# Kernel optimization log

Measured on AMD Instinct MI355X. Metric: run time of the kernel, lower is better.

The kernel has to match this reference:

```python
import jax, jax.numpy as jnp
import numpy as np

LN_EPS = 1e-5

def setup_inputs() -> dict:
    key = jax.random.key(0)
    ks = jax.random.split(key, 8)
    B, L, D, H = 4, 2048, 512, 8
    x = jax.random.normal(ks[0], (B, L, D), dtype=jnp.float32)
    token_ids = jax.random.randint(ks[1], (B, L), 0, 50000, dtype=jnp.int64)
    s = 1.0 / np.sqrt(D)
    Wq = jax.random.normal(ks[2], (D, D), dtype=jnp.float32) * s
    Wk = jax.random.normal(ks[3], (D, D), dtype=jnp.float32) * s
    Wv = jax.random.normal(ks[4], (D, D), dtype=jnp.float32) * s
    Wo = jax.random.normal(ks[5], (D, D), dtype=jnp.float32) * s
    gamma = jnp.ones((D,), dtype=jnp.float32)
    beta = jnp.zeros((D,), dtype=jnp.float32)
    return {"x": x, "token_ids": token_ids, "Wq": Wq, "Wk": Wk,
            "Wv": Wv, "Wo": Wo, "gamma": gamma, "beta": beta}

def reference(x, token_ids, Wq, Wk, Wv, Wo, gamma, beta):
    B, L, D = x.shape
    H = 8
    Dh = D // H
    residual = x
    # Pre-LN
    mu = jnp.mean(x, axis=-1, keepdims=True)
    var = jnp.mean(jnp.square(x - mu), axis=-1, keepdims=True)
    xn = (x - mu) * jax.lax.rsqrt(var + LN_EPS) * gamma + beta
    # projections (torch Linear: y = x @ W.T), split heads -> [B,H,L,Dh]
    def proj(W):
        return jnp.einsum('bld,ed->ble', xn, W).reshape(B, L, H, Dh).transpose(0, 2, 1, 3)
    Q, K, V = proj(Wq), proj(Wk), proj(Wv)
    scale = jnp.sqrt(jnp.float32(Dh))
    scores = jnp.einsum('bhqd,bhkd->bhqk', Q, K) / scale  # [B,H,L,L]
    neg_inf = jnp.float32(-jnp.inf)
    causal = jnp.triu(jnp.ones((L, L), dtype=bool), k=1)           # [L,L]
    pad = (token_ids == 0)[:, None, None, :]                       # [B,1,1,L]
    scores = jnp.where(causal[None, None], neg_inf, scores)
    scores = jnp.where(pad, neg_inf, scores)
    all_masked = jnp.all(jnp.isinf(scores), axis=-1, keepdims=True)
    scores = jnp.where(all_masked, 0.0, scores)
    attn = jax.nn.softmax(scores, axis=-1)  # dropout is identity in eval
    out = jnp.einsum('bhqk,bhkd->bhqd', attn, V)
    out = out.transpose(0, 2, 1, 3).reshape(B, L, D)
    out = jnp.einsum('bld,ed->ble', out, Wo)
    return residual + out
```

## Files before the change

kernel.cpp:

```cpp
#include <hip/hip_runtime.h>
#include <math.h>

typedef unsigned short u16;
typedef unsigned int u32;
typedef unsigned long long u64;
typedef float f32x4 __attribute__((ext_vector_type(4)));
typedef __bf16 bf16x8 __attribute__((ext_vector_type(8)));
typedef __bf16 bf16x4 __attribute__((ext_vector_type(4)));

constexpr int Bc = 4, Lc = 2048, Dc = 512, Hc = 8, DHc = 64;
constexpr int NTOK = Bc * Lc;
constexpr float LN_EPS = 1e-5f;
constexpr int KS = 72;
constexpr int PS = 72;
constexpr float QSCALE = 0.125f * 1.44269504088896340736f;
constexpr float MNEG = -1e30f;

__device__ inline u16 bf_bits(float f) {
  return __builtin_bit_cast(u16, (__bf16)f);
}

__global__ __launch_bounds__(256) void prep_kernel(const float* __restrict__ s0,
                                                   const float* __restrict__ s1,
                                                   const float* __restrict__ s2,
                                                   const float* __restrict__ s3,
                                                   u16* __restrict__ d0,
                                                   u16* __restrict__ d1,
                                                   u16* __restrict__ d2,
                                                   u16* __restrict__ d3,
                                                   const int* __restrict__ tok,
                                                   u64* __restrict__ pm) {
  int bid = blockIdx.x;
  if (bid < 1024) {
    int mat = bid >> 8;
    int i = ((bid & 255) * 256 + threadIdx.x) * 4;
    const float* s = (mat == 0) ? s0 : (mat == 1) ? s1 : (mat == 2) ? s2 : s3;
    u16* d = (mat == 0) ? d0 : (mat == 1) ? d1 : (mat == 2) ? d2 : d3;
    float4 v = *(const float4*)&s[i];
    bf16x4 o;
    o[0] = (__bf16)v.x; o[1] = (__bf16)v.y; o[2] = (__bf16)v.z; o[3] = (__bf16)v.w;
    *(bf16x4*)&d[i] = o;
  } else {
    int wid = ((bid - 1024) * 256 + threadIdx.x) >> 6;
    int lane = threadIdx.x & 63;
    u64 m = __ballot(tok[(size_t)wid * 64 + lane] == 0);
    if (lane == 0) pm[wid] = m;
  }
}

__global__ __launch_bounds__(256) void ln_kernel(const float* __restrict__ x,
                                                 const float* __restrict__ gamma,
                                                 const float* __restrict__ beta,
                                                 u16* __restrict__ xn) {
  int wave = threadIdx.x >> 6;
  int lane = threadIdx.x & 63;
  int row  = blockIdx.x * 4 + wave;
  const float* xr = x + (size_t)row * Dc;
  float4 v0 = ((const float4*)xr)[lane * 2];
  float4 v1 = ((const float4*)xr)[lane * 2 + 1];
  float sum = v0.x + v0.y + v0.z + v0.w + v1.x + v1.y + v1.z + v1.w;
  float sq  = v0.x*v0.x + v0.y*v0.y + v0.z*v0.z + v0.w*v0.w
            + v1.x*v1.x + v1.y*v1.y + v1.z*v1.z + v1.w*v1.w;
  #pragma unroll
  for (int off = 32; off > 0; off >>= 1) {
    sum += __shfl_xor(sum, off);
    sq  += __shfl_xor(sq, off);
  }
  float mu = sum * (1.0f / Dc);
  float rs = rsqrtf(sq * (1.0f / Dc) - mu * mu + LN_EPS);
  float4 g0 = ((const float4*)gamma)[lane * 2];
  float4 g1 = ((const float4*)gamma)[lane * 2 + 1];
  float4 b0 = ((const float4*)beta)[lane * 2];
  float4 b1 = ((const float4*)beta)[lane * 2 + 1];
  bf16x8 o;
  o[0] = (__bf16)((v0.x - mu) * rs * g0.x + b0.x);
  o[1] = (__bf16)((v0.y - mu) * rs * g0.y + b0.y);
  o[2] = (__bf16)((v0.z - mu) * rs * g0.z + b0.z);
  o[3] = (__bf16)((v0.w - mu) * rs * g0.w + b0.w);
  o[4] = (__bf16)((v1.x - mu) * rs * g1.x + b1.x);
  o[5] = (__bf16)((v1.y - mu) * rs * g1.y + b1.y);
  o[6] = (__bf16)((v1.z - mu) * rs * g1.z + b1.z);
  o[7] = (__bf16)((v1.w - mu) * rs * g1.w + b1.w);
  *(bf16x8*)&xn[(size_t)row * Dc + lane * 8] = o;
}

template <int MODE>
__global__ __launch_bounds__(256) void gemm_bf16(const u16* __restrict__ A,
                                                 const u16* __restrict__ W,
                                                 const float* __restrict__ res,
                                                 float* __restrict__ out_f,
                                                 u16* __restrict__ o_q,
                                                 u16* __restrict__ o_k,
                                                 u16* __restrict__ o_v,
                                                 float* __restrict__ vm) {
  __shared__ u16 As[128 * KS];
  __shared__ u16 Bs[128 * KS];
  int tid = threadIdx.x;
  int lane = tid & 63;
  int w = tid >> 6;
  int wr = w >> 1, wc = w & 1;
  int cc = lane & 15, rb = lane >> 4;
  int n0 = blockIdx.x * 128;
  int e0 = blockIdx.y * 128;
  f32x4 acc[4][4] = {};
  for (int k0 = 0; k0 < Dc; k0 += 64) {
    #pragma unroll
    for (int u = 0; u < 4; u++) {
      int idx = u * 256 + tid;
      int row = idx >> 3;
      int col = (idx & 7) << 3;
      *(uint4*)&As[row * KS + col] = *(const uint4*)&A[(size_t)(n0 + row) * Dc + k0 + col];
      *(uint4*)&Bs[row * KS + col] = *(const uint4*)&W[(size_t)(e0 + row) * Dc + k0 + col];
    }
    __syncthreads();
    #pragma unroll
    for (int kk = 0; kk < 64; kk += 32) {
      bf16x8 aF[4], bF[4];
      #pragma unroll
      for (int m = 0; m < 4; m++)
        aF[m] = *(bf16x8*)&As[(wr * 64 + m * 16 + cc) * KS + kk + rb * 8];
      #pragma unroll
      for (int n = 0; n < 4; n++)
        bF[n] = *(bf16x8*)&Bs[(wc * 64 + n * 16 + cc) * KS + kk + rb * 8];
      #pragma unroll
      for (int m = 0; m < 4; m++)
        #pragma unroll
        for (int n = 0; n < 4; n++)
          acc[m][n] = __builtin_amdgcn_mfma_f32_16x16x32_bf16(aF[m], bF[n], acc[m][n], 0, 0, 0);
    }
    __syncthreads();
  }
  if (MODE == 3) {
    int bb = n0 >> 11;
    int mat = e0 >> 9;
    int e0c = e0 & 511;
    if (mat == 2) {
      #pragma unroll
      for (int n = 0; n < 4; n++) {
        int c = e0c + wc * 64 + n * 16 + cc;
        int h = c >> 6, dh = c & 63;
        float cp = 0.f;
        #pragma unroll
        for (int m = 0; m < 4; m++) {
          int l = (n0 + wr * 64 + m * 16 + rb * 4) & (Lc - 1);
          bf16x4 o4;
          o4[0] = (__bf16)acc[m][n][0]; o4[1] = (__bf16)acc[m][n][1];
          o4[2] = (__bf16)acc[m][n][2]; o4[3] = (__bf16)acc[m][n][3];
          size_t addr = ((((size_t)(bb * Hc + h)) * (Lc / 64) + (l >> 6)) * DHc + dh) * 64 + (l & 63);
          *(bf16x4*)&o_v[addr] = o4;
          cp += (acc[m][n][0] + acc[m][n][1]) + (acc[m][n][2] + acc[m][n][3]);
        }
        cp += __shfl_xor(cp, 16);
        cp += __shfl_xor(cp, 32);
        if (lane < 16) atomicAdd(&vm[(bb * Hc + h) * DHc + dh], cp);
      }
    } else {
      float sc = (mat == 0) ? QSCALE : 1.0f;
      u16* dst = (mat == 0) ? o_q : o_k;
      #pragma unroll
      for (int m = 0; m < 4; m++) {
        #pragma unroll
        for (int n = 0; n < 4; n++) {
          #pragma unroll
          for (int j = 0; j < 4; j++) {
            int r = n0 + wr * 64 + m * 16 + rb * 4 + j;
            int c = e0c + wc * 64 + n * 16 + cc;
            int ll = r & (Lc - 1);
            dst[(((size_t)(bb * Hc + (c >> 6))) * Lc + ll) * DHc + (c & 63)] = bf_bits(acc[m][n][j] * sc);
          }
        }
      }
    }
  } else {
    #pragma unroll
    for (int m = 0; m < 4; m++) {
      #pragma unroll
      for (int n = 0; n < 4; n++) {
        #pragma unroll
        for (int j = 0; j < 4; j++) {
          int r = n0 + wr * 64 + m * 16 + rb * 4 + j;
          int c = e0 + wc * 64 + n * 16 + cc;
          size_t o = (size_t)r * Dc + c;
          out_f[o] = acc[m][n][j] + res[o];
        }
      }
    }
  }
}

__global__ __launch_bounds__(64) void attn11(const u16* __restrict__ Q,
                                             const u16* __restrict__ K,
                                             const u16* __restrict__ VT,
                                             const float* __restrict__ vm,
                                             const u64* __restrict__ pmask,
                                             u16* __restrict__ out) {
  __shared__ u16 Ps[32 * PS];
  int lane = threadIdx.x;
  int cc = lane & 15, rb = lane >> 4;
  int bh = blockIdx.x;
  int qt = (int)gridDim.y - 1 - (int)blockIdx.y;
  int q0 = qt * 32;
  int b = bh >> 3, h = bh & 7;
  const u16* Qb = Q + (size_t)bh * Lc * DHc;
  const u16* Kb = K + (size_t)bh * Lc * DHc;
  const u16* Vb = VT + (size_t)bh * Lc * DHc;
  const u64* pmb = pmask + (b << 5);
  int nfull = q0 >> 6;

  bf16x8 qF[2][2];
  #pragma unroll
  for (int qb = 0; qb < 2; qb++)
    #pragma unroll
    for (int kc = 0; kc < 2; kc++)
      qF[qb][kc] = *(const bf16x8*)&Qb[(size_t)(q0 + qb * 16 + cc) * DHc + kc * 32 + rb * 8];

  float mrow[2] = {MNEG, MNEG};
  float lrow[2] = {0.f, 0.f};
  f32x4 acc[2][4] = {};

  bf16x8 kfA[4][2], kfB[4][2];
  {
    const u16* kp = Kb;
    #pragma unroll
    for (int c = 0; c < 4; c++) {
      kfA[c][0] = *(const bf16x8*)&kp[(c * 16 + cc) * DHc + rb * 8];
      kfA[c][1] = *(const bf16x8*)&kp[(c * 16 + cc) * DHc + 32 + rb * 8];
    }
  }
  if (nfull >= 1) {
    const u16* kp = Kb + (size_t)64 * DHc;
    #pragma unroll
    for (int c = 0; c < 4; c++) {
      kfB[c][0] = *(const bf16x8*)&kp[(c * 16 + cc) * DHc + rb * 8];
      kfB[c][1] = *(const bf16x8*)&kp[(c * 16 + cc) * DHc + 32 + rb * 8];
    }
  }

  auto body = [&](int kt, bf16x8 (&kf)[4][2]) {
    int k0 = kt * 64;
    bool last = (kt == nfull);
    u64 pm = pmb[kt];
    const u16* vp = Vb + (size_t)kt * (DHc * 64);
    bf16x8 vf[2][4];
    #pragma unroll
    for (int kc = 0; kc < 2; kc++)
      #pragma unroll
      for (int d0 = 0; d0 < 4; d0++)
        vf[kc][d0] = *(const bf16x8*)&vp[(d0 * 16 + cc) * 64 + kc * 32 + rb * 8];

    f32x4 sq[2][4] = {};
    __builtin_amdgcn_s_setprio(1);
    #pragma unroll
    for (int c = 0; c < 4; c++) {
      #pragma unroll
      for (int qb = 0; qb < 2; qb++) {
        sq[qb][c] = __builtin_amdgcn_mfma_f32_16x16x32_bf16(kf[c][0], qF[qb][0], sq[qb][c], 0, 0, 0);
        sq[qb][c] = __builtin_amdgcn_mfma_f32_16x16x32_bf16(kf[c][1], qF[qb][1], sq[qb][c], 0, 0, 0);
      }
    }
    __builtin_amdgcn_s_setprio(0);
    if (kt + 2 <= nfull) {
      const u16* kp = Kb + (size_t)(k0 + 128) * DHc;
      #pragma unroll
      for (int c = 0; c < 4; c++) {
        kf[c][0] = *(const bf16x8*)&kp[(c * 16 + cc) * DHc + rb * 8];
        kf[c][1] = *(const bf16x8*)&kp[(c * 16 + cc) * DHc + 32 + rb * 8];
      }
    }
    if (pm) {
      #pragma unroll
      for (int c = 0; c < 4; c++) {
        u32 smr = (((u32)(pm >> (c * 16)) & 0xffffu) >> (rb * 4));
        #pragma unroll
        for (int qb = 0; qb < 2; qb++)
          #pragma unroll
          for (int j = 0; j < 4; j++)
            if ((smr >> j) & 1) sq[qb][c][j] = -INFINITY;
      }
    }
    if (last) {
      #pragma unroll
      for (int qb = 0; qb < 2; qb++) {
        int qrel = q0 + qb * 16 + cc - k0;
        #pragma unroll
        for (int c = 0; c < 4; c++)
          #pragma unroll
          for (int j = 0; j < 4; j++)
            if (c * 16 + rb * 4 + j > qrel) sq[qb][c][j] = -INFINITY;
      }
    }
    #pragma unroll
    for (int qb = 0; qb < 2; qb++) {
      float m0 = fmaxf(fmaxf(sq[qb][0][0], sq[qb][0][1]), fmaxf(sq[qb][0][2], sq[qb][0][3]));
      float m1 = fmaxf(fmaxf(sq[qb][1][0], sq[qb][1][1]), fmaxf(sq[qb][1][2], sq[qb][1][3]));
      float m2 = fmaxf(fmaxf(sq[qb][2][0], sq[qb][2][1]), fmaxf(sq[qb][2][2], sq[qb][2][3]));
      float m3 = fmaxf(fmaxf(sq[qb][3][0], sq[qb][3][1]), fmaxf(sq[qb][3][2], sq[qb][3][3]));
      float mx = fmaxf(fmaxf(m0, m1), fmaxf(m2, m3));
      mx = fmaxf(mx, __shfl_xor(mx, 16));
      mx = fmaxf(mx, __shfl_xor(mx, 32));
      if (!__all(mx <= mrow[qb] + 8.f)) {
        float nm = fmaxf(mrow[qb], mx);
        float alpha = exp2f(mrow[qb] - nm);
        lrow[qb] *= alpha;
        #pragma unroll
        for (int d0 = 0; d0 < 4; d0++)
          #pragma unroll
          for (int j = 0; j < 4; j++)
            acc[qb][d0][j] *= alpha;
        mrow[qb] = nm;
      }
      float rs = 0.f;
      #pragma unroll
      for (int c = 0; c < 4; c++) {
        f32x4 p;
        #pragma unroll
        for (int j = 0; j < 4; j++) p[j] = exp2f(sq[qb][c][j] - mrow[qb]);
        rs += (p[0] + p[1]) + (p[2] + p[3]);
        bf16x4 p4;
        p4[0] = (__bf16)p[0]; p4[1] = (__bf16)p[1];
        p4[2] = (__bf16)p[2]; p4[3] = (__bf16)p[3];
        *(bf16x4*)&Ps[(qb * 16 + cc) * PS + c * 16 + rb * 4] = p4;
      }
      rs += __shfl_xor(rs, 16);
      rs += __shfl_xor(rs, 32);
      lrow[qb] += rs;
    }
    asm volatile("s_waitcnt lgkmcnt(0)" ::: "memory");
    __builtin_amdgcn_sched_barrier(0);
    __builtin_amdgcn_s_setprio(1);
    #pragma unroll
    for (int kc = 0; kc < 2; kc++) {
      bf16x8 pF0 = *(bf16x8*)&Ps[(size_t)cc * PS + kc * 32 + rb * 8];
      bf16x8 pF1 = *(bf16x8*)&Ps[(size_t)(16 + cc) * PS + kc * 32 + rb * 8];
      #pragma unroll
      for (int d0 = 0; d0 < 4; d0++) {
        acc[0][d0] = __builtin_amdgcn_mfma_f32_16x16x32_bf16(vf[kc][d0], pF0, acc[0][d0], 0, 0, 0);
        acc[1][d0] = __builtin_amdgcn_mfma_f32_16x16x32_bf16(vf[kc][d0], pF1, acc[1][d0], 0, 0, 0);
      }
    }
    __builtin_amdgcn_s_setprio(0);
  };

  for (int kt = 0; kt <= nfull; kt += 2) {
    body(kt, kfA);
    if (kt + 1 <= nfull) body(kt + 1, kfB);
  }

  #pragma unroll
  for (int qb = 0; qb < 2; qb++) {
    int q = q0 + qb * 16 + cc;
    bool ok = lrow[qb] > 0.f;
    float inv = ok ? 1.0f / lrow[qb] : 0.f;
    #pragma unroll
    for (int d0 = 0; d0 < 4; d0++) {
      bf16x4 o4;
      #pragma unroll
      for (int j = 0; j < 4; j++) {
        float v = ok ? acc[qb][d0][j] * inv
                     : vm[bh * DHc + d0 * 16 + rb * 4 + j] * (1.0f / Lc);
        o4[j] = (__bf16)v;
      }
      *(bf16x4*)&out[((size_t)(b * Lc + q)) * Dc + h * DHc + d0 * 16 + rb * 4] = o4;
    }
  }
}

extern "C" void kernel_launch(void* const* d_in, const int* in_sizes, int n_in,
                              void* d_out, int out_size, void* d_ws, size_t ws_size,
                              hipStream_t stream) {
  const float* x     = (const float*)d_in[0];
  const int*   tok   = (const int*)d_in[1];
  const float* Wq    = (const float*)d_in[2];
  const float* Wk    = (const float*)d_in[3];
  const float* Wv    = (const float*)d_in[4];
  const float* Wo    = (const float*)d_in[5];
  const float* gamma = (const float*)d_in[6];
  const float* beta  = (const float*)d_in[7];
  float* out = (float*)d_out;

  const size_t SEG = (size_t)NTOK * Dc;
  const size_t WSEG = (size_t)Dc * Dc;
  u16* xn   = (u16*)d_ws;
  u16* Qd   = xn + SEG;
  u16* Kd   = Qd + SEG;
  u16* VT   = Kd + SEG;
  u16* ao   = VT + SEG;
  u16* Wqkv = ao + SEG;
  u16* Wob  = Wqkv + 3 * WSEG;
  float* vm = (float*)(Wob + WSEG);
  u64* pmarr = (u64*)(vm + (size_t)Bc * Hc * DHc);

  (void)hipMemsetAsync(vm, 0, (size_t)Bc * Hc * DHc * sizeof(float), stream);

  prep_kernel<<<1056, 256, 0, stream>>>(Wq, Wk, Wv, Wo,
                                        Wqkv, Wqkv + WSEG, Wqkv + 2 * WSEG, Wob,
                                        tok, pmarr);
  ln_kernel<<<NTOK / 4, 256, 0, stream>>>(x, gamma, beta, xn);

  dim3 gq(NTOK / 128, (3 * Dc) / 128);
  gemm_bf16<3><<<gq, 256, 0, stream>>>(xn, Wqkv, nullptr, nullptr, Qd, Kd, VT, vm);

  dim3 ga(Bc * Hc, Lc / 32);
  attn11<<<ga, 64, 0, stream>>>(Qd, Kd, VT, vm, pmarr, ao);

  dim3 gg(NTOK / 128, Dc / 128);
  gemm_bf16<0><<<gg, 256, 0, stream>>>(ao, Wob, x, out, nullptr, nullptr, nullptr, nullptr);
}
```

Baseline: 120.2 us.

## Double-buffer GEMM tiles via direct global-to-LDS loads and fuse prep, LN, memset

The bf16 GEMM now double-buffers its A/W tiles in LDS, using global_load_lds direct copies with an XOR swizzle in place of padded rows. The next k-tile is fetched while the current one is consumed, hiding global load latency behind MFMA work. Separately, the weight conversion, pad-mask ballot, vm zeroing and LayerNorm are merged into one launch, and the hipMemsetAsync is dropped, removing two launches. Risks: the hand-written vmcnt waits and barrier placement must match the load counts exactly, and the doubled LDS use may lower occupancy.

Result: faster. 106.5 us (-11.4%).

```diff
diff --git a/kernel.cpp b/kernel.cpp
--- a/kernel.cpp
+++ b/kernel.cpp
@@ -11,7 +11,6 @@
 constexpr int Bc = 4, Lc = 2048, Dc = 512, Hc = 8, DHc = 64;
 constexpr int NTOK = Bc * Lc;
 constexpr float LN_EPS = 1e-5f;
-constexpr int KS = 72;
 constexpr int PS = 72;
 constexpr float QSCALE = 0.125f * 1.44269504088896340736f;
 constexpr float MNEG = -1e30f;
@@ -20,16 +19,21 @@
   return __builtin_bit_cast(u16, (__bf16)f);
 }
 
-__global__ __launch_bounds__(256) void prep_kernel(const float* __restrict__ s0,
-                                                   const float* __restrict__ s1,
-                                                   const float* __restrict__ s2,
-                                                   const float* __restrict__ s3,
-                                                   u16* __restrict__ d0,
-                                                   u16* __restrict__ d1,
-                                                   u16* __restrict__ d2,
-                                                   u16* __restrict__ d3,
-                                                   const int* __restrict__ tok,
-                                                   u64* __restrict__ pm) {
+__global__ __launch_bounds__(256) void prep2_kernel(const float* __restrict__ s0,
+                                                    const float* __restrict__ s1,
+                                                    const float* __restrict__ s2,
+                                                    const float* __restrict__ s3,
+                                                    u16* __restrict__ d0,
+                                                    u16* __restrict__ d1,
+                                                    u16* __restrict__ d2,
+                                                    u16* __restrict__ d3,
+                                                    const int* __restrict__ tok,
+                                                    u64* __restrict__ pm,
+                                                    float* __restrict__ vm,
+                                                    const float* __restrict__ x,
+                                                    const float* __restrict__ gamma,
+                                                    const float* __restrict__ beta,
+                                                    u16* __restrict__ xn) {
   int bid = blockIdx.x;
   if (bid < 1024) {
     int mat = bid >> 8;
@@ -40,48 +44,48 @@
     bf16x4 o;
     o[0] = (__bf16)v.x; o[1] = (__bf16)v.y; o[2] = (__bf16)v.z; o[3] = (__bf16)v.w;
     *(bf16x4*)&d[i] = o;
-  } else {
+  } else if (bid < 1056) {
     int wid = ((bid - 1024) * 256 + threadIdx.x) >> 6;
     int lane = threadIdx.x & 63;
     u64 m = __ballot(tok[(size_t)wid * 64 + lane] == 0);
     if (lane == 0) pm[wid] = m;
-  }
-}
-
-__global__ __launch_bounds__(256) void ln_kernel(const float* __restrict__ x,
-                                                 const float* __restrict__ gamma,
-                                                 const float* __restrict__ beta,
-                                                 u16* __restrict__ xn) {
-  int wave = threadIdx.x >> 6;
-  int lane = threadIdx.x & 63;
-  int row  = blockIdx.x * 4 + wave;
-  const float* xr = x + (size_t)row * Dc;
-  float4 v0 = ((const float4*)xr)[lane * 2];
-  float4 v1 = ((const float4*)xr)[lane * 2 + 1];
-  float sum = v0.x + v0.y + v0.z + v0.w + v1.x + v1.y + v1.z + v1.w;
-  float sq  = v0.x*v0.x + v0.y*v0.y + v0.z*v0.z + v0.w*v0.w
-            + v1.x*v1.x + v1.y*v1.y + v1.z*v1.z + v1.w*v1.w;
-  #pragma unroll
-  for (int off = 32; off > 0; off >>= 1) {
-    sum += __shfl_xor(sum, off);
-    sq  += __shfl_xor(sq, off);
-  }
-  float mu = sum * (1.0f / Dc);
-  float rs = rsqrtf(sq * (1.0f / Dc) - mu * mu + LN_EPS);
-  float4 g0 = ((const float4*)gamma)[lane * 2];
-  float4 g1 = ((const float4*)gamma)[lane * 2 + 1];
-  float4 b0 = ((const float4*)beta)[lane * 2];
-  float4 b1 = ((const float4*)beta)[lane * 2 + 1];
-  bf16x8 o;
-  o[0] = (__bf16)((v0.x - mu) * rs * g0.x + b0.x);
-  o[1] = (__bf16)((v0.y - mu) * rs * g0.y + b0.y);
-  o[2] = (__bf16)((v0.z - mu) * rs * g0.z + b0.z);
-  o[3] = (__bf16)((v0.w - mu) * rs * g0.w + b0.w);
-  o[4] = (__bf16)((v1.x - mu) * rs * g1.x + b1.x);
-  o[5] = (__bf16)((v1.y - mu) * rs * g1.y + b1.y);
-  o[6] = (__bf16)((v1.z - mu) * rs * g1.z + b1.z);
-  o[7] = (__bf16)((v1.w - mu) * rs * g1.w + b1.w);
-  *(bf16x8*)&xn[(size_t)row * Dc + lane * 8] = o;
+    if (bid == 1024) {
+      float4 z = make_float4(0.f, 0.f, 0.f, 0.f);
+      *(float4*)&vm[threadIdx.x * 8] = z;
+      *(float4*)&vm[threadIdx.x * 8 + 4] = z;
+    }
+  } else {
+    int wave = threadIdx.x >> 6;
+    int lane = threadIdx.x & 63;
+    int row  = (bid - 1056) * 4 + wave;
+    const float* xr = x + (size_t)row * Dc;
+    float4 v0 = ((const float4*)xr)[lane * 2];
+    float4 v1 = ((const float4*)xr)[lane * 2 + 1];
+    float sum = v0.x + v0.y + v0.z + v0.w + v1.x + v1.y + v1.z + v1.w;
+    float sq  = v0.x*v0.x + v0.y*v0.y + v0.z*v0.z + v0.w*v0.w
+              + v1.x*v1.x + v1.y*v1.y + v1.z*v1.z + v1.w*v1.w;
+    #pragma unroll
+    for (int off = 32; off > 0; off >>= 1) {
+      sum += __shfl_xor(sum, off);
+      sq  += __shfl_xor(sq, off);
+    }
+    float mu = sum * (1.0f / Dc);
+    float rs = rsqrtf(sq * (1.0f / Dc) - mu * mu + LN_EPS);
+    float4 g0 = ((const float4*)gamma)[lane * 2];
+    float4 g1 = ((const float4*)gamma)[lane * 2 + 1];
+    float4 b0 = ((const float4*)beta)[lane * 2];
+    float4 b1 = ((const float4*)beta)[lane * 2 + 1];
+    bf16x8 o;
+    o[0] = (__bf16)((v0.x - mu) * rs * g0.x + b0.x);
+    o[1] = (__bf16)((v0.y - mu) * rs * g0.y + b0.y);
+    o[2] = (__bf16)((v0.z - mu) * rs * g0.z + b0.z);
+    o[3] = (__bf16)((v0.w - mu) * rs * g0.w + b0.w);
+    o[4] = (__bf16)((v1.x - mu) * rs * g1.x + b1.x);
+    o[5] = (__bf16)((v1.y - mu) * rs * g1.y + b1.y);
+    o[6] = (__bf16)((v1.z - mu) * rs * g1.z + b1.z);
+    o[7] = (__bf16)((v1.w - mu) * rs * g1.w + b1.w);
+    *(bf16x8*)&xn[(size_t)row * Dc + lane * 8] = o;
+  }
 }
 
 template <int MODE>
@@ -93,8 +97,8 @@
                                                  u16* __restrict__ o_k,
                                                  u16* __restrict__ o_v,
                                                  float* __restrict__ vm) {
-  __shared__ u16 As[128 * KS];
-  __shared__ u16 Bs[128 * KS];
+  __shared__ u16 As[2][128 * 64];
+  __shared__ u16 Bs[2][128 * 64];
   int tid = threadIdx.x;
   int lane = tid & 63;
   int w = tid >> 6;
@@ -102,26 +106,52 @@
   int cc = lane & 15, rb = lane >> 4;
   int n0 = blockIdx.x * 128;
   int e0 = blockIdx.y * 128;
+
+  auto stage = [&](int k0, int buf) {
+    #pragma unroll
+    for (int i = 0; i < 4; i++) {
+      int s = (i * 4 + w) * 64 + lane;
+      int row = s >> 3;
+      int colp = (s & 7) ^ (row & 7);
+      const char* gA = (const char*)&A[(size_t)(n0 + row) * Dc + k0] + colp * 16;
+      const char* gB = (const char*)&W[(size_t)(e0 + row) * Dc + k0] + colp * 16;
+      __builtin_amdgcn_global_load_lds(
+          (const __attribute__((address_space(1))) void*)gA,
+          (__attribute__((address_space(3))) void*)&As[buf][(i * 4 + w) * 512], 16, 0, 0);
+      __builtin_amdgcn_global_load_lds(
+          (const __attribute__((address_space(1))) void*)gB,
+          (__attribute__((address_space(3))) void*)&Bs[buf][(i * 4 + w) * 512], 16, 0, 0);
+    }
+  };
+
   f32x4 acc[4][4] = {};
-  for (int k0 = 0; k0 < Dc; k0 += 64) {
-    #pragma unroll
-    for (int u = 0; u < 4; u++) {
-      int idx = u * 256 + tid;
-      int row = idx >> 3;
-      int col = (idx & 7) << 3;
-      *(uint4*)&As[row * KS + col] = *(const uint4*)&A[(size_t)(n0 + row) * Dc + k0 + col];
-      *(uint4*)&Bs[row * KS + col] = *(const uint4*)&W[(size_t)(e0 + row) * Dc + k0 + col];
-    }
-    __syncthreads();
-    #pragma unroll
-    for (int kk = 0; kk < 64; kk += 32) {
+  stage(0, 0);
+  for (int kt = 0; kt < 8; kt++) {
+    int cur = kt & 1;
+    if (kt < 7) {
+      stage((kt + 1) << 6, cur ^ 1);
+      asm volatile("s_waitcnt vmcnt(8)" ::: "memory");
+    } else {
+      asm volatile("s_waitcnt vmcnt(0)" ::: "memory");
+    }
+    __builtin_amdgcn_sched_barrier(0);
+    __builtin_amdgcn_s_barrier();
+    __builtin_amdgcn_sched_barrier(0);
+    #pragma unroll
+    for (int kk = 0; kk < 2; kk++) {
       bf16x8 aF[4], bF[4];
       #pragma unroll
-      for (int m = 0; m < 4; m++)
-        aF[m] = *(bf16x8*)&As[(wr * 64 + m * 16 + cc) * KS + kk + rb * 8];
-      #pragma unroll
-      for (int n = 0; n < 4; n++)
-        bF[n] = *(bf16x8*)&Bs[(wc * 64 + n * 16 + cc) * KS + kk + rb * 8];
+      for (int m = 0; m < 4; m++) {
+        int row = wr * 64 + m * 16 + cc;
+        int cp = ((rb + kk * 4) ^ (cc & 7)) << 3;
+        aF[m] = *(bf16x8*)&As[cur][row * 64 + cp];
+      }
+      #pragma unroll
+      for (int n = 0; n < 4; n++) {
+        int row = wc * 64 + n * 16 + cc;
+        int cp = ((rb + kk * 4) ^ (cc & 7)) << 3;
+        bF[n] = *(bf16x8*)&Bs[cur][row * 64 + cp];
+      }
       #pragma unroll
       for (int m = 0; m < 4; m++)
         #pragma unroll
@@ -130,6 +160,7 @@
     }
     __syncthreads();
   }
+
   if (MODE == 3) {
     int bb = n0 >> 11;
     int mat = e0 >> 9;
@@ -390,12 +421,9 @@
   float* vm = (float*)(Wob + WSEG);
   u64* pmarr = (u64*)(vm + (size_t)Bc * Hc * DHc);
 
-  (void)hipMemsetAsync(vm, 0, (size_t)Bc * Hc * DHc * sizeof(float), stream);
-
-  prep_kernel<<<1056, 256, 0, stream>>>(Wq, Wk, Wv, Wo,
-                                        Wqkv, Wqkv + WSEG, Wqkv + 2 * WSEG, Wob,
-                                        tok, pmarr);
-  ln_kernel<<<NTOK / 4, 256, 0, stream>>>(x, gamma, beta, xn);
+  prep2_kernel<<<3104, 256, 0, stream>>>(Wq, Wk, Wv, Wo,
+                                         Wqkv, Wqkv + WSEG, Wqkv + 2 * WSEG, Wob,
+                                         tok, pmarr, vm, x, gamma, beta, xn);
 
   dim3 gq(NTOK / 128, (3 * Dc) / 128);
   gemm_bf16<3><<<gq, 256, 0, stream>>>(xn, Wqkv, nullptr, nullptr, Qd, Kd, VT, vm);
```
